# Kernel tuning notes

Hardware: AMD Instinct MI355X
Metric: run time of the kernel (lower is better)

Reference implementation:

```python
import jax, jax.numpy as jnp
import numpy as np

EPS = 1e-10


def setup_inputs() -> dict:
    key = jax.random.key(0)
    k1, k2 = jax.random.split(key)
    B, C, H, W = 8, 16, 512, 512
    x = jax.random.normal(k1, (B, C, H, W), dtype=jnp.float32)
    # grid_sample-style normalized coordinates in [-1, 1]
    inv_grid = jax.random.uniform(k2, (B, H, W, 2), dtype=jnp.float32, minval=-1.0, maxval=1.0)
    return {"x": x, "inv_grid": inv_grid}


def reference(x, inv_grid):
    # Inverse bilinear splat: scatter-add each input pixel into the 4 nearest
    # output cells with bilinear weights. OH = OW = None -> output HxW = input HxW.
    B, C, H, W = x.shape
    h, w = H, W
    g = (inv_grid + 1.0) * 0.5
    gi = jnp.clip(g[..., 0] * h + 1.0, 0.0, h + 1 - 2 * EPS)  # (B,H,W)
    gj = jnp.clip(g[..., 1] * w + 1.0, 0.0, w + 1 - 2 * EPS)
    # values are >= 0, so trunc (torch .long()) == floor
    fi = jnp.floor(gi).astype(jnp.int32)
    fj = jnp.floor(gj).astype(jnp.int32)

    A = jnp.zeros((B, C, h + 3, w + 3), dtype=x.dtype)
    b_idx = jnp.arange(B, dtype=jnp.int32)[:, None, None]  # broadcasts to (B,H,W)
    vals = jnp.moveaxis(x, 1, -1)  # (B,H,W,C) -- weights are shared across channels

    for di in (0, 1):
        wi = jax.nn.relu(1.0 - jnp.abs(gi - (fi + di).astype(gi.dtype)))
        for dj in (0, 1):
            wj = jax.nn.relu(1.0 - jnp.abs(gj - (fj + dj).astype(gj.dtype)))
            wgt = (wi * wj)[..., None]  # (B,H,W,1)
            # mixed advanced indexing: result gathers to (B,H,W,C); duplicates accumulate
            A = A.at[b_idx, :, fi + di, fj + dj].add(vals * wgt)

    return A[..., 1:h + 1, 1:w + 1]
```

## Files before the change

### kernel.cpp

```cpp
#include <hip/hip_runtime.h>
#include <stdint.h>

#define BB 8
#define CC 16
#define HH 512
#define WW 512
#define HW (HH * WW)
#define NPIX (BB * HW)

#define TS 8
#define TI 64
#define TJ 64
#define NBINS (BB * TI * TJ)
#define NCOPY 4
#define NSUB (NBINS * NCOPY)
#define CAP_SUB 96
#define CSTRIDE 100

__device__ __forceinline__ uint32_t bf16_rne(float f) {
    uint32_t u = __float_as_uint(f);
    return (u + 0x7fffu + ((u >> 16) & 1u)) >> 16;
}

struct Dec { int oi0, oj0; unsigned wbits; };
__device__ __forceinline__ Dec decode(float gx, float gy) {
    float gi = ((gx + 1.0f) * 0.5f) * (float)HH + 1.0f;
    float gj = ((gy + 1.0f) * 0.5f) * (float)WW + 1.0f;
    gi = fminf(fmaxf(gi, 0.0f), (float)(HH + 1));
    gj = fminf(fmaxf(gj, 0.0f), (float)(WW + 1));
    int fi = (int)gi, fj = (int)gj;
    float ai = gi - (float)fi;
    float aj = gj - (float)fj;
    Dec d;
    d.oi0 = fi - 1;
    d.oj0 = fj - 1;
    unsigned aq = (unsigned)(ai * 1023.0f + 0.5f);
    unsigned bq = (unsigned)(aj * 1023.0f + 0.5f);
    d.wbits = (aq << 10) | bq;
    return d;
}

__global__ __launch_bounds__(256) void k_init(unsigned* __restrict__ cursors) {
    int i = blockIdx.x * 256 + threadIdx.x;
    cursors[i] = (unsigned)i * CAP_SUB;
}

__global__ __launch_bounds__(256) void k_scatter(const float* __restrict__ x,
                                                 const float2* __restrict__ grid,
                                                 unsigned* __restrict__ cursors,
                                                 uint32_t* __restrict__ vals8,
                                                 uint2* __restrict__ recs) {
    __shared__ uint32_t st[256 * 8];
    int tid = threadIdx.x;
    int idx = blockIdx.x * 256 + tid;
    float2 g = grid[idx];
    int b = idx >> 18;
    Dec d = decode(g.x, g.y);

    const float* xp = x + (size_t)b * CC * HW + (idx & (HW - 1));
#pragma unroll
    for (int q = 0; q < 8; ++q) {
        float a = xp[(2 * q) * HW];
        float bb = xp[(2 * q + 1) * HW];
        st[tid * 8 + q] = bf16_rne(a) | (bf16_rne(bb) << 16);
    }
    __syncthreads();
    {
        uint4* vg = (uint4*)vals8 + (size_t)blockIdx.x * 512;
        const uint4* sv = (const uint4*)st;
        vg[tid]       = sv[tid];
        vg[tid + 256] = sv[tid + 256];
    }

    if (d.oi0 >= HH || d.oj0 >= WW) return;
    int bI = d.oi0 >> 3, bJ = d.oj0 >> 3;
    int sub = d.oi0 & 3;
    unsigned si = (unsigned)(d.oi0 & 7) + 1;
    unsigned sj = (unsigned)(d.oj0 & 7) + 1;
    bool vr = (si == 8) && (d.oi0 != HH - 1);
    bool vc = (sj == 8) && (d.oj0 != WW - 1);
    auto emit = [&](int bi, int bj, unsigned s10) {
        unsigned sidx = (unsigned)((((b * TI + bi) << 6) + bj) * NCOPY + sub);
        unsigned slot = atomicAdd(&cursors[sidx], 1u);
        if (slot < sidx * CAP_SUB + CAP_SUB)
            recs[slot] = make_uint2(d.wbits, (s10 << 21) | (unsigned)idx);
    };
    emit(bI, bJ, si * 10 + sj);
    if (vr) emit(bI + 1, bJ, sj);
    if (vc) emit(bI, bJ + 1, si * 10);
    if (vr && vc) emit(bI + 1, bJ + 1, 0);
}

__global__ __launch_bounds__(256) void k_accum(const uint32_t* __restrict__ vals8,
                                               const uint2* __restrict__ recs,
                                               const unsigned* __restrict__ cursors,
                                               float* __restrict__ out) {
    __shared__ float acc[4][CC * CSTRIDE];
    int wid = threadIdx.x >> 6;
    int lane = threadIdx.x & 63;
    int bin = blockIdx.x * 4 + wid;
    float* A = acc[wid];

    for (int k = lane; k < CC * CSTRIDE; k += 64) A[k] = 0.0f;

    uint4 cur = ((const uint4*)cursors)[bin];

    int ch = lane >> 2, tap = lane & 3;
    int di = tap >> 1, dj = tap & 1;
    float swi = (di ? 1.0f : -1.0f) * (1.0f / 1023.0f);
    float ci  = di ? 0.0f : 1.0f;
    float swj = (dj ? 1.0f : -1.0f) * (1.0f / 1023.0f);
    float cj  = dj ? 0.0f : 1.0f;
    int sh = (ch & 1) ? 0 : 16;
    int laneconst = ch * CSTRIDE + di * 10 + dj;
    const uint32_t* vw = vals8 + (lane >> 3);

#pragma unroll
    for (int s = 0; s < NCOPY; ++s) {
        unsigned sidx = (unsigned)(bin * NCOPY + s);
        unsigned base = sidx * CAP_SUB;
        unsigned cend = (s == 0) ? cur.x : (s == 1) ? cur.y : (s == 2) ? cur.z : cur.w;
        unsigned n = (unsigned)__builtin_amdgcn_readfirstlane((int)(cend - base));
        if (n > CAP_SUB) n = CAP_SUB;
        if (n == 0) continue;
        unsigned nm1 = n - 1;
        const uint2* mp = recs + base;

        for (unsigned it = 0; it < n; it += 8) {
            uint2 mr[8];
#pragma unroll
            for (int r = 0; r < 8; ++r) {
                unsigned j = it + r;
                mr[r] = mp[j > nm1 ? nm1 : j];
            }
            uint32_t vv[8];
#pragma unroll
            for (int r = 0; r < 8; ++r)
                vv[r] = vw[(mr[r].y & 0x1FFFFFu) * 8u];
#pragma unroll
            for (int r = 0; r < 8; ++r) {
                unsigned m = mr[r].x;
                unsigned s10 = mr[r].y >> 21;
                float aif = (float)((m >> 10) & 1023u);
                float ajf = (float)(m & 1023u);
                float wi = fmaf(swi, aif, ci);
                float wj = fmaf(swj, ajf, cj);
                float w = (it + r <= nm1) ? wi * wj : 0.0f;
                float vf = __uint_as_float((vv[r] << sh) & 0xffff0000u);
                A[laneconst + (int)s10] += vf * w;
            }
        }
    }

    int tj = bin & 63, ti = (bin >> 6) & 63, b = bin >> 12;
    int gi0 = ti * TS, gj0 = tj * TS;
    int row = lane >> 3, col = lane & 7;
    for (int c = 0; c < CC; ++c) {
        float v = A[c * CSTRIDE + (row + 1) * 10 + (col + 1)];
        out[((size_t)(b * CC + c) * HH + gi0 + row) * WW + gj0 + col] = v;
    }
}

__global__ __launch_bounds__(256) void splat_kernel(const float* __restrict__ x,
                                                    const float* __restrict__ grid,
                                                    float* __restrict__ out) {
    int idx = blockIdx.x * 256 + threadIdx.x;
    int j = idx & (WW - 1);
    int i = (idx >> 9) & (HH - 1);
    int b = idx >> 18;
    float2 g2 = reinterpret_cast<const float2*>(grid)[idx];
    float gi = ((g2.x + 1.0f) * 0.5f) * (float)HH + 1.0f;
    float gj = ((g2.y + 1.0f) * 0.5f) * (float)WW + 1.0f;
    gi = fminf(fmaxf(gi, 0.0f), (float)(HH + 1));
    gj = fminf(fmaxf(gj, 0.0f), (float)(WW + 1));
    int fi = (int)gi, fj = (int)gj;
    float ai = gi - (float)fi, aj = gj - (float)fj;
    float wi0 = 1.0f - ai, wj0 = 1.0f - aj;
    float w00 = wi0 * wj0, w01 = wi0 * aj, w10 = ai * wj0, w11 = ai * aj;
    int oi0 = fi - 1, oj0 = fj - 1;
    bool vi0 = (oi0 < HH), vi1 = (fi < HH), vj0 = (oj0 < WW), vj1 = (fj < WW);
    const float* xp = x + (size_t)b * CC * HW + i * WW + j;
    float* op = out + (size_t)b * CC * HW + oi0 * WW + oj0;
#pragma unroll
    for (int ch = 0; ch < CC; ++ch) {
        float v = xp[ch * HW];
        float* o = op + ch * HW;
        if (vi0 & vj0) unsafeAtomicAdd(o, v * w00);
        if (vi0 & vj1) unsafeAtomicAdd(o + 1, v * w01);
        if (vi1 & vj0) unsafeAtomicAdd(o + WW, v * w10);
        if (vi1 & vj1) unsafeAtomicAdd(o + WW + 1, v * w11);
    }
}

extern "C" void kernel_launch(void* const* d_in, const int* in_sizes, int n_in,
                              void* d_out, int out_size, void* d_ws, size_t ws_size,
                              hipStream_t stream) {
    const float* x = (const float*)d_in[0];
    const float* grid = (const float*)d_in[1];
    float* out = (float*)d_out;

    const size_t vals_bytes = (size_t)NPIX * 32;
    const size_t recs_bytes = (size_t)NSUB * CAP_SUB * 8;
    const size_t cur_bytes  = (size_t)NSUB * 4;
    const size_t need = vals_bytes + recs_bytes + cur_bytes + 256;

    if (ws_size < need) {
        hipMemsetAsync(out, 0, (size_t)out_size * sizeof(float), stream);
        splat_kernel<<<NPIX / 256, 256, 0, stream>>>(x, grid, out);
        return;
    }

    char* ws = (char*)d_ws;
    uint32_t* vals8   = (uint32_t*)ws;                        ws += vals_bytes;
    uint2*    recs    = (uint2*)ws;                           ws += recs_bytes;
    unsigned* cursors = (unsigned*)ws;

    const float2* grid2 = (const float2*)grid;
    k_init<<<NSUB / 256, 256, 0, stream>>>(cursors);
    k_scatter<<<NPIX / 256, 256, 0, stream>>>(x, grid2, cursors, vals8, recs);
    k_accum<<<NBINS / 4, 256, 0, stream>>>(vals8, recs, cursors, out);
}
```

Measured before the change: 274.7 us.

## Pack four 8-bit bilinear weights per record and software-prefetch record batches

The scatter kernel now precomputes the four bilinear tap weights, quantizes each to 8 bits and packs them into one word. The accumulate kernel extracts its tap's byte instead of rebuilding weights from 10-bit fractions with FMAs. The record loop also double-buffers its loads so the next batch of 8 records is fetched while the current one is processed. This trims per-record ALU work and hides record-load latency. The cost is coarser weight precision (8-bit instead of two 10-bit fractions) and extra registers for the second buffer.

```diff
diff --git a/kernel.cpp b/kernel.cpp
--- a/kernel.cpp
+++ b/kernel.cpp
@@ -22,21 +22,18 @@
     return (u + 0x7fffu + ((u >> 16) & 1u)) >> 16;
 }
 
-struct Dec { int oi0, oj0; unsigned wbits; };
+struct Dec { int oi0, oj0; float ai, aj; };
 __device__ __forceinline__ Dec decode(float gx, float gy) {
     float gi = ((gx + 1.0f) * 0.5f) * (float)HH + 1.0f;
     float gj = ((gy + 1.0f) * 0.5f) * (float)WW + 1.0f;
     gi = fminf(fmaxf(gi, 0.0f), (float)(HH + 1));
     gj = fminf(fmaxf(gj, 0.0f), (float)(WW + 1));
     int fi = (int)gi, fj = (int)gj;
-    float ai = gi - (float)fi;
-    float aj = gj - (float)fj;
     Dec d;
+    d.ai = gi - (float)fi;
+    d.aj = gj - (float)fj;
     d.oi0 = fi - 1;
     d.oj0 = fj - 1;
-    unsigned aq = (unsigned)(ai * 1023.0f + 0.5f);
-    unsigned bq = (unsigned)(aj * 1023.0f + 0.5f);
-    d.wbits = (aq << 10) | bq;
     return d;
 }
 
@@ -79,11 +76,20 @@
     unsigned sj = (unsigned)(d.oj0 & 7) + 1;
     bool vr = (si == 8) && (d.oi0 != HH - 1);
     bool vc = (sj == 8) && (d.oj0 != WW - 1);
+
+    float wi0 = 1.0f - d.ai, wi1 = d.ai;
+    float wj0 = 1.0f - d.aj, wj1 = d.aj;
+    unsigned q00 = (unsigned)fmaf(wi0 * wj0, 255.0f, 0.5f);
+    unsigned q01 = (unsigned)fmaf(wi0 * wj1, 255.0f, 0.5f);
+    unsigned q10 = (unsigned)fmaf(wi1 * wj0, 255.0f, 0.5f);
+    unsigned q11 = (unsigned)fmaf(wi1 * wj1, 255.0f, 0.5f);
+    unsigned wpack = q00 | (q01 << 8) | (q10 << 16) | (q11 << 24);
+
     auto emit = [&](int bi, int bj, unsigned s10) {
         unsigned sidx = (unsigned)((((b * TI + bi) << 6) + bj) * NCOPY + sub);
         unsigned slot = atomicAdd(&cursors[sidx], 1u);
         if (slot < sidx * CAP_SUB + CAP_SUB)
-            recs[slot] = make_uint2(d.wbits, (s10 << 21) | (unsigned)idx);
+            recs[slot] = make_uint2(wpack, (s10 << 21) | (unsigned)idx);
     };
     emit(bI, bJ, si * 10 + sj);
     if (vr) emit(bI + 1, bJ, sj);
@@ -107,10 +113,7 @@
 
     int ch = lane >> 2, tap = lane & 3;
     int di = tap >> 1, dj = tap & 1;
-    float swi = (di ? 1.0f : -1.0f) * (1.0f / 1023.0f);
-    float ci  = di ? 0.0f : 1.0f;
-    float swj = (dj ? 1.0f : -1.0f) * (1.0f / 1023.0f);
-    float cj  = dj ? 0.0f : 1.0f;
+    int wsh = tap << 3;
     int sh = (ch & 1) ? 0 : 16;
     int laneconst = ch * CSTRIDE + di * 10 + dj;
     const uint32_t* vw = vals8 + (lane >> 3);
@@ -126,29 +129,32 @@
         unsigned nm1 = n - 1;
         const uint2* mp = recs + base;
 
+        uint2 mrA[8], mrB[8];
+#pragma unroll
+        for (int r = 0; r < 8; ++r) {
+            unsigned j = (unsigned)r;
+            mrA[r] = mp[j > nm1 ? nm1 : j];
+        }
         for (unsigned it = 0; it < n; it += 8) {
-            uint2 mr[8];
 #pragma unroll
             for (int r = 0; r < 8; ++r) {
-                unsigned j = it + r;
-                mr[r] = mp[j > nm1 ? nm1 : j];
+                unsigned j = it + 8 + r;
+                mrB[r] = mp[j > nm1 ? nm1 : j];
             }
             uint32_t vv[8];
 #pragma unroll
             for (int r = 0; r < 8; ++r)
-                vv[r] = vw[(mr[r].y & 0x1FFFFFu) * 8u];
+                vv[r] = vw[(mrA[r].y & 0x1FFFFFu) * 8u];
 #pragma unroll
             for (int r = 0; r < 8; ++r) {
-                unsigned m = mr[r].x;
-                unsigned s10 = mr[r].y >> 21;
-                float aif = (float)((m >> 10) & 1023u);
-                float ajf = (float)(m & 1023u);
-                float wi = fmaf(swi, aif, ci);
-                float wj = fmaf(swj, ajf, cj);
-                float w = (it + r <= nm1) ? wi * wj : 0.0f;
+                unsigned s10 = mrA[r].y >> 21;
+                float wb = (float)((mrA[r].x >> wsh) & 255u);
                 float vf = __uint_as_float((vv[r] << sh) & 0xffff0000u);
-                A[laneconst + (int)s10] += vf * w;
+                float vfs = (it + r <= nm1) ? vf * (1.0f / 255.0f) : 0.0f;
+                A[laneconst + (int)s10] += vfs * wb;
             }
+#pragma unroll
+            for (int r = 0; r < 8; ++r) mrA[r] = mrB[r];
         }
     }
 
```

New measurement: 302.7 us. 1.1x slower.
